# Kernel tuning notes

Hardware: AMD Instinct MI355X
Metric: run time of the kernel (lower is better)

## Reference

```python
import jax, jax.numpy as jnp
import numpy as np

H = 128; L = 4; N_TOTAL = 2500; M = 4; K = 12
S = N_TOTAL * M          # 10000 subgraphs
F = S * K                # 120000 flat nodes
E_INTRA = 2 * F          # 240000 intra-subgraph edges
E_INTER = 16 * N_TOTAL   # 40000 canonical edges
B = 50; VOCAB = 119; MAX_DIST = 32; BN_EPS = 1e-5


def _bn(x, g, b):
    # training-mode BatchNorm1d over rows (biased var, eps=1e-5)
    mu = x.mean(0)
    var = x.var(0)
    return (x - mu) * jax.lax.rsqrt(var + BN_EPS) * g + b


def _gine(x, ei, ea, W1, b1, W2, b2):
    # PyG GINEConv, eps=0: MLP(x + sum_{src->dst} relu(x[src] + e))
    msg = jax.nn.relu(x[ei[0]] + ea)                              # [E,H]
    agg = jax.ops.segment_sum(msg, ei[1], num_segments=x.shape[0])
    h = x + agg
    return jax.nn.relu(h @ W1 + b1) @ W2 + b2


def setup_inputs():
    key = jax.random.key(0)
    ks = list(jax.random.split(key, 32)); it = iter(ks)
    nk = lambda: next(it)
    rn = lambda shape, s=0.05: jax.random.normal(nk(), shape, dtype=jnp.float32) * s
    x_tok = jax.random.randint(nk(), (F,), 0, VOCAB)
    dist = jax.random.randint(nk(), (F,), 0, MAX_DIST + 1)
    node_ids = jax.random.randint(nk(), (F,), 0, N_TOTAL)
    node_ids = jnp.where(jax.random.uniform(nk(), (F,)) < 0.1, -1, node_ids)
    root_flat_idx = jnp.arange(S) * K
    node_ids = node_ids.at[root_flat_idx].set(jnp.arange(S) // M)  # root = canonical node
    valid = node_ids >= 0
    sub_batch = jnp.repeat(jnp.arange(S), K)
    src = jax.random.randint(nk(), (E_INTRA,), 0, F)
    dst = (src // K) * K + jax.random.randint(nk(), (E_INTRA,), 0, K)  # stay inside subgraph
    intra_ei = jnp.stack([src, dst])
    edge_index = jax.random.randint(nk(), (2, E_INTER), 0, N_TOTAL)
    batch_ids = jnp.arange(N_TOTAL) // (N_TOTAL // B)
    lp = -jax.random.uniform(nk(), (S,)) * 3.0                    # log-probs <= 0
    z = lambda *shape: jnp.zeros(shape, jnp.float32)
    o = lambda *shape: jnp.ones(shape, jnp.float32)
    return dict(
        x_tok=x_tok, dist=dist, node_ids=node_ids, valid=valid,
        sub_batch=sub_batch, root_flat_idx=root_flat_idx,
        intra_ei=intra_ei, edge_index=edge_index, batch_ids=batch_ids,
        lp=lp, ea_flat=rn((E_INTRA, H)), edge_attr=rn((E_INTER, H)),
        atom_emb=rn((VOCAB, H)), dist_emb=rn((MAX_DIST + 1, H)),
        logp_w=rn((1, H)), logp_b=z(H),
        intra_W1=rn((L, H, H)), intra_b1=z(L, H),
        intra_W2=rn((L, H, H)), intra_b2=z(L, H),
        intra_bn_g=o(L, H), intra_bn_b=z(L, H),
        self_W=rn((L, H, H)), self_b=z(L, H),
        root_W=rn((L, H, H)), root_b=z(L, H),
        inter_W1=rn((L, H, H)), inter_b1=z(L, H),
        inter_W2=rn((L, H, H)), inter_b2=z(L, H),
        inter_bn_g=o(L, H), inter_bn_b=z(L, H),
        readout_bn_g=o(H), readout_bn_b=z(H),
        alpha_pool=o(1), alpha_inter=o(1),
    )


def reference(x_tok, dist, node_ids, valid, sub_batch, root_flat_idx, intra_ei,
              edge_index, batch_ids, lp, ea_flat, edge_attr, atom_emb, dist_emb,
              logp_w, logp_b, intra_W1, intra_b1, intra_W2, intra_b2,
              intra_bn_g, intra_bn_b, self_W, self_b, root_W, root_b,
              inter_W1, inter_b1, inter_W2, inter_b2, inter_bn_g, inter_bn_b,
              readout_bn_g, readout_bn_b, alpha_pool, alpha_inter):
    valid_f = valid.astype(jnp.float32)[:, None]                  # [F,1]
    is_root_f = jnp.zeros((F, 1), jnp.float32).at[root_flat_idx].set(1.0)
    clamped_ids = jnp.maximum(node_ids, 0)
    # input encoding: atom embedding + BFS-distance PE + log-prob PE
    logp_pe = jax.nn.relu(lp[sub_batch][:, None] * logp_w[0] + logp_b)
    h = (atom_emb[x_tok] + dist_emb[dist] + logp_pe) * valid_f
    # HT inter-root weights, normalized per canonical root id
    root_ids = node_ids[root_flat_idx]                            # [S]
    rv = root_ids >= 0
    rid = jnp.maximum(root_ids, 0)
    w_un = jnp.where(rv, jnp.exp(-alpha_inter[0] * lp), 0.0)
    w_sum = jax.ops.segment_sum(w_un, rid, num_segments=N_TOTAL)
    ht_w = jnp.where(rv, w_un / (w_sum[rid] + 1e-16), 0.0)        # [S]
    for l in range(L):
        h1 = _gine(h, intra_ei, ea_flat, intra_W1[l], intra_b1[l], intra_W2[l], intra_b2[l])
        h1 = _bn(h1, intra_bn_g[l], intra_bn_b[l]) * valid_f
        h_root_bcast = h[sub_batch * K]
        h_non_root = (h @ self_W[l] + self_b[l]) + (h_root_bcast @ root_W[l] + root_b[l])
        # HT-weighted scatter of root reps to canonical nodes
        h_roots = h[root_flat_idx]                                # [S,H]
        h_root_canon = jax.ops.segment_sum(h_roots * ht_w[:, None], rid, num_segments=N_TOTAL)
        h_inter = _gine(h_root_canon, edge_index, edge_attr, inter_W1[l], inter_b1[l], inter_W2[l], inter_b2[l])
        h_inter = _bn(h_inter, inter_bn_g[l], inter_bn_b[l])
        h_inter_bcast = h_inter[clamped_ids] * valid_f
        out = is_root_f * (h1 + h_inter_bcast) + (1.0 - is_root_f) * (h1 + h_non_root)
        h = jax.nn.relu(out) * valid_f                            # dropout p=0
    # HT softmax readout over the m subgraphs of each canonical node
    h_sub = jax.ops.segment_sum(h * valid_f, sub_batch, num_segments=S)
    h_sub_2d = h_sub.reshape(N_TOTAL, M, H)
    w = jax.nn.softmax(-alpha_pool[0] * lp.reshape(N_TOTAL, M), axis=1)
    node_emb = jnp.einsum('nm,nmh->nh', w, h_sub_2d)
    node_emb = _bn(node_emb, readout_bn_g, readout_bn_b)
    return jax.ops.segment_sum(node_emb, batch_ids, num_segments=B)  # [B,H]
```

## Files before the change

### kernel.cpp

```cpp
#include <hip/hip_runtime.h>
#include <math.h>

#define H 128
#define H4 (H/4)
#define KK 12
#define MSUB 4
#define FF 120000
#define SS 10000
#define NN 2500
#define NBATCH 50
#define NLAYER 4
#define EINTRA 240000
#define EINTER 40000
#define HH (H*H)
#define BN_EPS 1e-5f
#define CAP_I 32
#define CAP_E 96

typedef short short8 __attribute__((ext_vector_type(8)));
typedef float floatx4 __attribute__((ext_vector_type(4)));

__device__ __forceinline__ unsigned short f2bf_rne(float x){
  unsigned u = __float_as_uint(x);
  unsigned r = u + 0x7FFFu + ((u >> 16) & 1u);
  return (unsigned short)(r >> 16);
}


__global__ void k_zero(float* __restrict__ p, int n){
  int i = blockIdx.x*256 + threadIdx.x;
  if (i < n) p[i] = 0.f;
}

__global__ void k_zeroi(int* __restrict__ p, int n){
  int i = blockIdx.x*256 + threadIdx.x;
  if (i < n) p[i] = 0;
}


__global__ void k_bucket(const int* __restrict__ dst, int E, int* __restrict__ cnt,
                         int* __restrict__ beid, int cap){
  int e = blockIdx.x*256 + threadIdx.x;
  if (e >= E) return;
  int d = dst[e];
  int p = atomicAdd(&cnt[d], 1);
  if (p < cap) beid[(size_t)d*cap + p] = e;
}


__global__ void k_encode(float* __restrict__ h, const int* __restrict__ xtok,
                         const int* __restrict__ dist, const int* __restrict__ nids,
                         const int* __restrict__ subb, const float* __restrict__ lp,
                         const float* __restrict__ aemb, const float* __restrict__ demb,
                         const float* __restrict__ lw, const float* __restrict__ lb){
  int idx = blockIdx.x*256 + threadIdx.x;
  if (idx >= FF*H4) return;
  int f = idx >> 5; int c = (idx & 31) << 2;
  float vf = (nids[f] >= 0) ? 1.f : 0.f;
  float l = lp[subb[f]];
  float4 a = *(const float4*)(aemb + (size_t)xtok[f]*H + c);
  float4 d = *(const float4*)(demb + (size_t)dist[f]*H + c);
  float4 w = *(const float4*)(lw + c);
  float4 b = *(const float4*)(lb + c);
  float4 o;
  o.x = (a.x + d.x + fmaxf(fmaf(l, w.x, b.x), 0.f)) * vf;
  o.y = (a.y + d.y + fmaxf(fmaf(l, w.y, b.y), 0.f)) * vf;
  o.z = (a.z + d.z + fmaxf(fmaf(l, w.z, b.z), 0.f)) * vf;
  o.w = (a.w + d.w + fmaxf(fmaf(l, w.w, b.w), 0.f)) * vf;
  *(float4*)(h + (size_t)f*H + c) = o;
}


__global__ void k_htw(const int* __restrict__ nids, const int* __restrict__ rfi,
                      const float* __restrict__ lp, const float* __restrict__ alpha,
                      float* __restrict__ htw){
  int n = blockIdx.x*256 + threadIdx.x;
  if (n >= NN) return;
  float a = alpha[0];
  float w[MSUB]; float sum = 0.f;
  #pragma unroll
  for (int m = 0; m < MSUB; ++m){
    int s = n*MSUB + m;
    int rid = nids[rfi[s]];
    float wm = (rid >= 0) ? expf(-a*lp[s]) : 0.f;
    w[m] = wm; sum += wm;
  }
  float inv = 1.f / (sum + 1e-16f);
  #pragma unroll
  for (int m = 0; m < MSUB; ++m) htw[n*MSUB + m] = w[m]*inv;
}


__global__ void k_gine_gather(float* __restrict__ outa, const float* __restrict__ x,
                              const float* __restrict__ ea, const int* __restrict__ cnt,
                              const int* __restrict__ beid, const int* __restrict__ src,
                              int rows, int cap){
  int idx = blockIdx.x*256 + threadIdx.x;
  if (idx >= rows*H4) return;
  int f = idx >> 5; int c = (idx & 31) << 2;
  float4 acc = *(const float4*)(x + (size_t)f*H + c);
  int n = cnt[f]; if (n > cap) n = cap;
  const int* bl = beid + (size_t)f*cap;
  for (int i = 0; i < n; ++i){
    int e = bl[i];
    int s = src[e];
    float4 xv = *(const float4*)(x + (size_t)s*H + c);
    float4 ev = *(const float4*)(ea + (size_t)e*H + c);
    acc.x += fmaxf(xv.x + ev.x, 0.f);
    acc.y += fmaxf(xv.y + ev.y, 0.f);
    acc.z += fmaxf(xv.z + ev.z, 0.f);
    acc.w += fmaxf(xv.w + ev.w, 0.f);
  }
  *(float4*)(outa + (size_t)f*H + c) = acc;
}


__global__ void k_canon(float* __restrict__ canon, const float* __restrict__ h,
                        const float* __restrict__ htw, const int* __restrict__ rfi){
  int idx = blockIdx.x*256 + threadIdx.x;
  if (idx >= NN*H4) return;
  int n = idx >> 5; int c = (idx & 31) << 2;
  float4 acc = make_float4(0.f,0.f,0.f,0.f);
  #pragma unroll
  for (int m = 0; m < MSUB; ++m){
    int s = n*MSUB + m;
    float w = htw[s];
    const float* p = h + (size_t)rfi[s]*H + c;
    acc.x += w*p[0]; acc.y += w*p[1]; acc.z += w*p[2]; acc.w += w*p[3];
  }
  *(float4*)(canon + (size_t)n*H + c) = acc;
}


__global__ __launch_bounds__(256, 2) void k_mm_mfma(
    const float* __restrict__ in, float* __restrict__ out, int rows,
    const float* __restrict__ W, const float* __restrict__ bias,
    int do_relu, const int* __restrict__ gather)
{
  __shared__ __align__(16) short wfrag[2][4][8][64][8];
  int tid = threadIdx.x;
  int w = tid >> 6, l = tid & 63;
  int quad = l >> 4, n15 = l & 15;

  #pragma unroll
  for (int i = 0; i < 8; ++i){
    int c = w + (i << 2);
    int ks = c >> 3, nt = c & 7;
    #pragma unroll
    for (int j = 0; j < 8; ++j){
      int k = ks*32 + quad*8 + j;
      int n = nt*16 + n15;
      float v = W[(size_t)k*H + n];
      unsigned short hb = f2bf_rne(v);
      float hf = __uint_as_float((unsigned)hb << 16);
      unsigned short lb = f2bf_rne(v - hf);
      wfrag[0][ks][nt][l][j] = (short)hb;
      wfrag[1][ks][nt][l][j] = (short)lb;
    }
  }
  __syncthreads();

  int ngroups = (rows + 63) >> 6;
  for (int g = blockIdx.x; g < ngroups; g += gridDim.x){
    int rload = g*64 + w*16 + n15;
    bool okload = rload < rows;
    int ir = okload ? (gather ? gather[rload] : rload) : 0;
    const float* ap = in + (size_t)ir*H + quad*8;

    short8 ah[4], al[4];
    #pragma unroll
    for (int ks = 0; ks < 4; ++ks){
      float4 a0 = okload ? *(const float4*)(ap + ks*32 + 0) : make_float4(0.f,0.f,0.f,0.f);
      float4 a1 = okload ? *(const float4*)(ap + ks*32 + 4) : make_float4(0.f,0.f,0.f,0.f);
      float av[8] = {a0.x,a0.y,a0.z,a0.w,a1.x,a1.y,a1.z,a1.w};
      #pragma unroll
      for (int j = 0; j < 8; ++j){
        unsigned short hb = f2bf_rne(av[j]);
        float hf = __uint_as_float((unsigned)hb << 16);
        ah[ks][j] = (short)hb;
        al[ks][j] = (short)f2bf_rne(av[j] - hf);
      }
    }

    floatx4 acc[8] = {};
    #pragma unroll
    for (int ks = 0; ks < 4; ++ks){
      #pragma unroll
      for (int nt = 0; nt < 8; ++nt){
        short8 bh = *(const short8*)&wfrag[0][ks][nt][l][0];
        short8 bl = *(const short8*)&wfrag[1][ks][nt][l][0];
        acc[nt] = __builtin_amdgcn_mfma_f32_16x16x32_bf16(ah[ks], bh, acc[nt], 0, 0, 0);
        acc[nt] = __builtin_amdgcn_mfma_f32_16x16x32_bf16(al[ks], bh, acc[nt], 0, 0, 0);
        acc[nt] = __builtin_amdgcn_mfma_f32_16x16x32_bf16(ah[ks], bl, acc[nt], 0, 0, 0);
      }
    }

    int rbase = g*64 + w*16 + quad*4;
    #pragma unroll
    for (int nt = 0; nt < 8; ++nt){
      int col = nt*16 + n15;
      float bv = bias[col];
      #pragma unroll
      for (int reg = 0; reg < 4; ++reg){
        int r = rbase + reg;
        if (r < rows){
          float v = acc[nt][reg] + bv;
          if (do_relu) v = fmaxf(v, 0.f);
          out[(size_t)r*H + col] = v;
        }
      }
    }
  }
}


__global__ void k_bnstats(const float* __restrict__ x, int rows, double* __restrict__ stats){
  int g = blockIdx.x*256 + threadIdx.x;
  int c = g & (H-1);
  int rstart = g >> 7;
  int rstride = (gridDim.x*256) >> 7;
  double s = 0.0, s2 = 0.0;
  for (int r = rstart; r < rows; r += rstride){
    float v = x[(size_t)r*H + c];
    s += v; s2 += (double)v*(double)v;
  }
  atomicAdd(&stats[c], s);
  atomicAdd(&stats[H+c], s2);
}

__global__ void k_bnfin(double* __restrict__ stats, int rows, float* __restrict__ muinv){
  int c = threadIdx.x;
  if (c < H){
    double mu = stats[c] / (double)rows;
    double var = stats[H+c] / (double)rows - mu*mu;
    muinv[c]   = (float)mu;
    muinv[H+c] = (float)(1.0 / sqrt(var + (double)BN_EPS));
    stats[c] = 0.0; stats[H+c] = 0.0;
  }
}

__global__ void k_bnapply(float* __restrict__ x, const float* __restrict__ muinv,
                          const float* __restrict__ g, const float* __restrict__ b, int rows){
  int idx = blockIdx.x*256 + threadIdx.x;
  if (idx >= rows*H4) return;
  int r = idx >> 5; int c = (idx & 31) << 2;
  float4 v  = *(const float4*)(x + (size_t)r*H + c);
  float4 mu = *(const float4*)(muinv + c);
  float4 iv = *(const float4*)(muinv + H + c);
  float4 gg = *(const float4*)(g + c);
  float4 bb = *(const float4*)(b + c);
  v.x = (v.x-mu.x)*iv.x*gg.x + bb.x;
  v.y = (v.y-mu.y)*iv.y*gg.y + bb.y;
  v.z = (v.z-mu.z)*iv.z*gg.z + bb.z;
  v.w = (v.w-mu.w)*iv.w*gg.w + bb.w;
  *(float4*)(x + (size_t)r*H + c) = v;
}


__global__ void k_combine(float* __restrict__ h, const float* __restrict__ h1raw,
                          const float* __restrict__ r1, const float* __restrict__ r2,
                          const float* __restrict__ hinter, const float* __restrict__ muinv,
                          const float* __restrict__ bg, const float* __restrict__ bb,
                          const int* __restrict__ nids){
  int idx = blockIdx.x*256 + threadIdx.x;
  if (idx >= FF*H4) return;
  int f = idx >> 5; int c = (idx & 31) << 2;
  int nid = nids[f];
  float vf = (nid >= 0) ? 1.f : 0.f;
  int cid = (nid < 0) ? 0 : nid;
  float4 x  = *(const float4*)(h1raw + (size_t)f*H + c);
  float4 mu = *(const float4*)(muinv + c);
  float4 iv = *(const float4*)(muinv + H + c);
  float4 g4 = *(const float4*)(bg + c);
  float4 b4 = *(const float4*)(bb + c);
  float4 h1;
  h1.x = ((x.x-mu.x)*iv.x*g4.x + b4.x) * vf;
  h1.y = ((x.y-mu.y)*iv.y*g4.y + b4.y) * vf;
  h1.z = ((x.z-mu.z)*iv.z*g4.z + b4.z) * vf;
  h1.w = ((x.w-mu.w)*iv.w*g4.w + b4.w) * vf;
  float4 o;
  if (f % KK == 0){
    float4 hi = *(const float4*)(hinter + (size_t)cid*H + c);
    o.x = h1.x + hi.x*vf; o.y = h1.y + hi.y*vf; o.z = h1.z + hi.z*vf; o.w = h1.w + hi.w*vf;
  } else {
    float4 a  = *(const float4*)(r1 + (size_t)f*H + c);
    float4 rr = *(const float4*)(r2 + (size_t)(f/KK)*H + c);
    o.x = h1.x + a.x + rr.x; o.y = h1.y + a.y + rr.y; o.z = h1.z + a.z + rr.z; o.w = h1.w + a.w + rr.w;
  }
  o.x = fmaxf(o.x,0.f)*vf; o.y = fmaxf(o.y,0.f)*vf; o.z = fmaxf(o.z,0.f)*vf; o.w = fmaxf(o.w,0.f)*vf;
  *(float4*)(h + (size_t)f*H + c) = o;
}


__global__ void k_hsub(float* __restrict__ hsub, const float* __restrict__ h){
  int idx = blockIdx.x*256 + threadIdx.x;
  if (idx >= SS*H4) return;
  int s = idx >> 5; int c = (idx & 31) << 2;
  float4 acc = make_float4(0.f,0.f,0.f,0.f);
  const float* base = h + (size_t)s*KK*H + c;
  #pragma unroll
  for (int k = 0; k < KK; ++k){
    float4 v = *(const float4*)(base + (size_t)k*H);
    acc.x += v.x; acc.y += v.y; acc.z += v.z; acc.w += v.w;
  }
  *(float4*)(hsub + (size_t)s*H + c) = acc;
}

__global__ void k_poolw(float* __restrict__ poolw, const float* __restrict__ lp,
                        const float* __restrict__ alpha){
  int n = blockIdx.x*256 + threadIdx.x;
  if (n >= NN) return;
  float a = alpha[0];
  float s0 = -a*lp[n*MSUB+0], s1 = -a*lp[n*MSUB+1], s2 = -a*lp[n*MSUB+2], s3 = -a*lp[n*MSUB+3];
  float m = fmaxf(fmaxf(s0,s1), fmaxf(s2,s3));
  float e0 = expf(s0-m), e1 = expf(s1-m), e2 = expf(s2-m), e3 = expf(s3-m);
  float sum = e0+e1+e2+e3;
  poolw[n*MSUB+0] = e0/sum; poolw[n*MSUB+1] = e1/sum;
  poolw[n*MSUB+2] = e2/sum; poolw[n*MSUB+3] = e3/sum;
}

__global__ void k_nodeemb(float* __restrict__ nemb, const float* __restrict__ hsub,
                          const float* __restrict__ poolw){
  int idx = blockIdx.x*256 + threadIdx.x;
  if (idx >= NN*H4) return;
  int n = idx >> 5; int c = (idx & 31) << 2;
  float w0 = poolw[n*MSUB+0], w1 = poolw[n*MSUB+1], w2 = poolw[n*MSUB+2], w3 = poolw[n*MSUB+3];
  const float* base = hsub + (size_t)n*MSUB*H + c;
  float4 v0 = *(const float4*)(base + 0*H);
  float4 v1 = *(const float4*)(base + 1*H);
  float4 v2 = *(const float4*)(base + 2*H);
  float4 v3 = *(const float4*)(base + 3*H);
  float4 o;
  o.x = w0*v0.x + w1*v1.x + w2*v2.x + w3*v3.x;
  o.y = w0*v0.y + w1*v1.y + w2*v2.y + w3*v3.y;
  o.z = w0*v0.z + w1*v1.z + w2*v2.z + w3*v3.z;
  o.w = w0*v0.w + w1*v1.w + w2*v2.w + w3*v3.w;
  *(float4*)(nemb + (size_t)n*H + c) = o;
}

__global__ void k_out(float* __restrict__ out, const float* __restrict__ nemb,
                      const float* __restrict__ muinv, const float* __restrict__ g,
                      const float* __restrict__ b){
  int idx = blockIdx.x*256 + threadIdx.x;
  if (idx >= NBATCH*H) return;
  int bi = idx >> 7; int c = idx & (H-1);
  float mu = muinv[c], iv = muinv[H+c], gg = g[c], bb = b[c];
  float acc = 0.f;
  const float* base = nemb + (size_t)bi*(NN/NBATCH)*H + c;
  for (int i = 0; i < NN/NBATCH; ++i)
    acc += (base[(size_t)i*H] - mu)*iv*gg + bb;
  out[idx] = acc;
}


extern "C" void kernel_launch(void* const* d_in, const int* in_sizes, int n_in,
                              void* d_out, int out_size, void* d_ws, size_t ws_size,
                              hipStream_t stream) {
  const int*   x_tok      = (const int*)  d_in[0];
  const int*   dist       = (const int*)  d_in[1];
  const int*   node_ids   = (const int*)  d_in[2];
  const int*   sub_batch  = (const int*)  d_in[4];
  const int*   rfi        = (const int*)  d_in[5];
  const int*   intra_ei   = (const int*)  d_in[6];
  const int*   edge_index = (const int*)  d_in[7];
  const float* lp         = (const float*)d_in[9];
  const float* ea_flat    = (const float*)d_in[10];
  const float* edge_attr  = (const float*)d_in[11];
  const float* atom_emb   = (const float*)d_in[12];
  const float* dist_emb   = (const float*)d_in[13];
  const float* logp_w     = (const float*)d_in[14];
  const float* logp_b     = (const float*)d_in[15];
  const float* intra_W1   = (const float*)d_in[16];
  const float* intra_b1   = (const float*)d_in[17];
  const float* intra_W2   = (const float*)d_in[18];
  const float* intra_b2   = (const float*)d_in[19];
  const float* intra_bn_g = (const float*)d_in[20];
  const float* intra_bn_b = (const float*)d_in[21];
  const float* self_W     = (const float*)d_in[22];
  const float* self_b     = (const float*)d_in[23];
  const float* root_W     = (const float*)d_in[24];
  const float* root_b     = (const float*)d_in[25];
  const float* inter_W1   = (const float*)d_in[26];
  const float* inter_b1   = (const float*)d_in[27];
  const float* inter_W2   = (const float*)d_in[28];
  const float* inter_b2   = (const float*)d_in[29];
  const float* inter_bn_g = (const float*)d_in[30];
  const float* inter_bn_b = (const float*)d_in[31];
  const float* ro_bn_g    = (const float*)d_in[32];
  const float* ro_bn_b    = (const float*)d_in[33];
  const float* alpha_pool = (const float*)d_in[34];
  const float* alpha_inter= (const float*)d_in[35];

  const int* isrc = intra_ei;
  const int* idst = intra_ei + EINTRA;
  const int* esrc = edge_index;
  const int* edst = edge_index + EINTER;

  float* out = (float*)d_out;

  char* ws = (char*)d_ws;
  size_t off = 0;
  auto nxt = [&](size_t bytes) -> void* {
    void* p = ws + off;
    off += (bytes + 255) & ~(size_t)255;
    return p;
  };
  float*  h      = (float*) nxt((size_t)FF*H*4);
  float*  hmid   = (float*) nxt((size_t)FF*H*4);
  float*  tbuf   = (float*) nxt((size_t)FF*H*4);
  float*  r2     = (float*) nxt((size_t)SS*H*4);
  float*  canon  = (float*) nxt((size_t)NN*H*4);
  float*  agg2   = (float*) nxt((size_t)NN*H*4);
  float*  hsub   = (float*) nxt((size_t)SS*H*4);
  float*  nemb   = (float*) nxt((size_t)NN*H*4);
  float*  htw    = (float*) nxt((size_t)SS*4);
  float*  poolw  = (float*) nxt((size_t)NN*MSUB*4);
  double* statsA = (double*)nxt((size_t)2*H*8);
  double* statsB = (double*)nxt((size_t)2*H*8);
  float*  muinvA = (float*) nxt((size_t)2*H*4);
  float*  muinvB = (float*) nxt((size_t)2*H*4);
  int*    icnt   = (int*)   nxt((size_t)FF*4);
  int*    ibeid  = (int*)   nxt((size_t)FF*CAP_I*4);
  int*    ecnt   = (int*)   nxt((size_t)NN*4);
  int*    ebeid  = (int*)   nxt((size_t)NN*CAP_E*4);
  (void)ws_size; (void)n_in; (void)in_sizes; (void)out_size; (void)sub_batch;

  const int G_FH4 = FF*H4/256;
  const int G_SH4 = SS*H4/256;
  const int G_NH4 = (NN*H4 + 255)/256;
  const int G_N   = (NN + 255)/256;
  const int G_MM_F = 512;
  const int G_MM_S = (SS + 63)/64;
  const int G_MM_N = (NN + 63)/64;

  k_zero<<<2, 256, 0, stream>>>((float*)statsA, 2*H*2);
  k_zero<<<2, 256, 0, stream>>>((float*)statsB, 2*H*2);
  k_zeroi<<<(FF+255)/256, 256, 0, stream>>>(icnt, FF);
  k_zeroi<<<G_N, 256, 0, stream>>>(ecnt, NN);

  k_bucket<<<(EINTRA+255)/256, 256, 0, stream>>>(idst, EINTRA, icnt, ibeid, CAP_I);
  k_bucket<<<(EINTER+255)/256, 256, 0, stream>>>(edst, EINTER, ecnt, ebeid, CAP_E);

  k_encode<<<G_FH4, 256, 0, stream>>>(h, x_tok, dist, node_ids, sub_batch, lp,
                                      atom_emb, dist_emb, logp_w, logp_b);
  k_htw<<<G_N, 256, 0, stream>>>(node_ids, rfi, lp, alpha_inter, htw);

  for (int l = 0; l < NLAYER; ++l){
    const float* W1 = intra_W1 + (size_t)l*HH; const float* b1 = intra_b1 + (size_t)l*H;
    const float* W2 = intra_W2 + (size_t)l*HH; const float* b2 = intra_b2 + (size_t)l*H;

    k_gine_gather<<<G_FH4, 256, 0, stream>>>(hmid, h, ea_flat, icnt, ibeid, isrc, FF, CAP_I);
    k_mm_mfma<<<G_MM_F, 256, 0, stream>>>(hmid, tbuf, FF, W1, b1, 1, nullptr);
    k_mm_mfma<<<G_MM_F, 256, 0, stream>>>(tbuf, hmid, FF, W2, b2, 0, nullptr);
    k_bnstats<<<512, 256, 0, stream>>>(hmid, FF, statsA);
    k_bnfin<<<1, 128, 0, stream>>>(statsA, FF, muinvA);

    k_canon<<<G_NH4, 256, 0, stream>>>(canon, h, htw, rfi);
    k_mm_mfma<<<G_MM_S, 256, 0, stream>>>(h, r2, SS, root_W + (size_t)l*HH,
                                          root_b + (size_t)l*H, 0, rfi);

    k_gine_gather<<<G_NH4, 256, 0, stream>>>(agg2, canon, edge_attr, ecnt, ebeid, esrc, NN, CAP_E);
    k_mm_mfma<<<G_MM_N, 256, 0, stream>>>(agg2, tbuf, NN, inter_W1 + (size_t)l*HH,
                                          inter_b1 + (size_t)l*H, 1, nullptr);
    k_mm_mfma<<<G_MM_N, 256, 0, stream>>>(tbuf, agg2, NN, inter_W2 + (size_t)l*HH,
                                          inter_b2 + (size_t)l*H, 0, nullptr);
    k_bnstats<<<128, 256, 0, stream>>>(agg2, NN, statsB);
    k_bnfin<<<1, 128, 0, stream>>>(statsB, NN, muinvB);
    k_bnapply<<<G_NH4, 256, 0, stream>>>(agg2, muinvB, inter_bn_g + (size_t)l*H,
                                         inter_bn_b + (size_t)l*H, NN);

    k_mm_mfma<<<G_MM_F, 256, 0, stream>>>(h, tbuf, FF, self_W + (size_t)l*HH,
                                          self_b + (size_t)l*H, 0, nullptr);
    k_combine<<<G_FH4, 256, 0, stream>>>(h, hmid, tbuf, r2, agg2, muinvA,
                                         intra_bn_g + (size_t)l*H,
                                         intra_bn_b + (size_t)l*H, node_ids);
  }

  k_hsub<<<G_SH4, 256, 0, stream>>>(hsub, h);
  k_poolw<<<G_N, 256, 0, stream>>>(poolw, lp, alpha_pool);
  k_nodeemb<<<G_NH4, 256, 0, stream>>>(nemb, hsub, poolw);
  k_bnstats<<<128, 256, 0, stream>>>(nemb, NN, statsB);
  k_bnfin<<<1, 128, 0, stream>>>(statsB, NN, muinvB);
  k_out<<<(NBATCH*H+255)/256, 256, 0, stream>>>(out, nemb, muinvB, ro_bn_g, ro_bn_b);
}
```

Before: 2.017 ms.

## Fuse self-matmul with combine epilogue and compact edge lists into CSR pairs

```diff
diff --git a/kernel.cpp b/kernel.cpp
--- a/kernel.cpp
+++ b/kernel.cpp
@@ -45,6 +45,41 @@
   int d = dst[e];
   int p = atomicAdd(&cnt[d], 1);
   if (p < cap) beid[(size_t)d*cap + p] = e;
+}
+
+__global__ void k_scan(const int* __restrict__ cnt, int rows, int cap,
+                       int* __restrict__ rowptr, int* __restrict__ gcount){
+  __shared__ int sdata[256];
+  __shared__ int sbase;
+  int tid = threadIdx.x;
+  int r = blockIdx.x*256 + tid;
+  int v = 0;
+  if (r < rows){ v = cnt[r]; if (v > cap) v = cap; }
+  sdata[tid] = v;
+  __syncthreads();
+  for (int ofs = 1; ofs < 256; ofs <<= 1){
+    int t = (tid >= ofs) ? sdata[tid-ofs] : 0;
+    __syncthreads();
+    sdata[tid] += t;
+    __syncthreads();
+  }
+  if (tid == 255) sbase = atomicAdd(gcount, sdata[255]);
+  __syncthreads();
+  if (r < rows) rowptr[r] = sbase + sdata[tid] - v;
+}
+
+__global__ void k_csr_fill(const int* __restrict__ cnt, const int* __restrict__ rowptr,
+                           const int* __restrict__ beid, const int* __restrict__ src,
+                           int rows, int cap, int2* __restrict__ es){
+  int f = blockIdx.x*256 + threadIdx.x;
+  if (f >= rows) return;
+  int n = cnt[f]; if (n > cap) n = cap;
+  int base = rowptr[f];
+  const int* bl = beid + (size_t)f*cap;
+  for (int i = 0; i < n; ++i){
+    int e = bl[i];
+    es[base + i] = make_int2(e, src[e]);
+  }
 }
 
 
@@ -91,25 +126,37 @@
 }
 
 
-__global__ void k_gine_gather(float* __restrict__ outa, const float* __restrict__ x,
-                              const float* __restrict__ ea, const int* __restrict__ cnt,
-                              const int* __restrict__ beid, const int* __restrict__ src,
-                              int rows, int cap){
+__global__ void k_gine_gather2(float* __restrict__ outa, const float* __restrict__ x,
+                               const float* __restrict__ ea, const int* __restrict__ cnt,
+                               const int* __restrict__ rowptr, const int2* __restrict__ es,
+                               int rows, int cap){
   int idx = blockIdx.x*256 + threadIdx.x;
   if (idx >= rows*H4) return;
   int f = idx >> 5; int c = (idx & 31) << 2;
   float4 acc = *(const float4*)(x + (size_t)f*H + c);
   int n = cnt[f]; if (n > cap) n = cap;
-  const int* bl = beid + (size_t)f*cap;
-  for (int i = 0; i < n; ++i){
-    int e = bl[i];
-    int s = src[e];
-    float4 xv = *(const float4*)(x + (size_t)s*H + c);
-    float4 ev = *(const float4*)(ea + (size_t)e*H + c);
-    acc.x += fmaxf(xv.x + ev.x, 0.f);
-    acc.y += fmaxf(xv.y + ev.y, 0.f);
-    acc.z += fmaxf(xv.z + ev.z, 0.f);
-    acc.w += fmaxf(xv.w + ev.w, 0.f);
+  const int2* p = es + rowptr[f];
+  int i = 0;
+  for (; i + 2 <= n; i += 2){
+    int2 e0 = p[i];
+    int2 e1 = p[i+1];
+    float4 x0 = *(const float4*)(x + (size_t)e0.y*H + c);
+    float4 a0 = *(const float4*)(ea + (size_t)e0.x*H + c);
+    float4 x1 = *(const float4*)(x + (size_t)e1.y*H + c);
+    float4 a1 = *(const float4*)(ea + (size_t)e1.x*H + c);
+    acc.x += fmaxf(x0.x + a0.x, 0.f) + fmaxf(x1.x + a1.x, 0.f);
+    acc.y += fmaxf(x0.y + a0.y, 0.f) + fmaxf(x1.y + a1.y, 0.f);
+    acc.z += fmaxf(x0.z + a0.z, 0.f) + fmaxf(x1.z + a1.z, 0.f);
+    acc.w += fmaxf(x0.w + a0.w, 0.f) + fmaxf(x1.w + a1.w, 0.f);
+  }
+  if (i < n){
+    int2 e0 = p[i];
+    float4 x0 = *(const float4*)(x + (size_t)e0.y*H + c);
+    float4 a0 = *(const float4*)(ea + (size_t)e0.x*H + c);
+    acc.x += fmaxf(x0.x + a0.x, 0.f);
+    acc.y += fmaxf(x0.y + a0.y, 0.f);
+    acc.z += fmaxf(x0.z + a0.z, 0.f);
+    acc.w += fmaxf(x0.w + a0.w, 0.f);
   }
   *(float4*)(outa + (size_t)f*H + c) = acc;
 }
@@ -207,6 +254,99 @@
           float v = acc[nt][reg] + bv;
           if (do_relu) v = fmaxf(v, 0.f);
           out[(size_t)r*H + col] = v;
+        }
+      }
+    }
+  }
+}
+
+
+__global__ __launch_bounds__(256, 2) void k_mm_combine(
+    const float* in, float* hout, int rows,
+    const float* __restrict__ W, const float* __restrict__ bias,
+    const float* __restrict__ hmid, const float* __restrict__ r2,
+    const float* __restrict__ hinter, const float* __restrict__ muinv,
+    const float* __restrict__ bng, const float* __restrict__ bnb,
+    const int* __restrict__ nids)
+{
+  __shared__ __align__(16) short wfrag[2][4][8][64][8];
+  int tid = threadIdx.x;
+  int w = tid >> 6, l = tid & 63;
+  int quad = l >> 4, n15 = l & 15;
+
+  #pragma unroll
+  for (int i = 0; i < 8; ++i){
+    int c = w + (i << 2);
+    int ks = c >> 3, nt = c & 7;
+    #pragma unroll
+    for (int j = 0; j < 8; ++j){
+      int k = ks*32 + quad*8 + j;
+      int n = nt*16 + n15;
+      float v = W[(size_t)k*H + n];
+      unsigned short hb = f2bf_rne(v);
+      float hf = __uint_as_float((unsigned)hb << 16);
+      unsigned short lb = f2bf_rne(v - hf);
+      wfrag[0][ks][nt][l][j] = (short)hb;
+      wfrag[1][ks][nt][l][j] = (short)lb;
+    }
+  }
+  __syncthreads();
+
+  int ngroups = (rows + 63) >> 6;
+  for (int g = blockIdx.x; g < ngroups; g += gridDim.x){
+    int rload = g*64 + w*16 + n15;
+    bool okload = rload < rows;
+    const float* ap = in + (size_t)(okload ? rload : 0)*H + quad*8;
+
+    short8 ah[4], al[4];
+    #pragma unroll
+    for (int ks = 0; ks < 4; ++ks){
+      float4 a0 = okload ? *(const float4*)(ap + ks*32 + 0) : make_float4(0.f,0.f,0.f,0.f);
+      float4 a1 = okload ? *(const float4*)(ap + ks*32 + 4) : make_float4(0.f,0.f,0.f,0.f);
+      float av[8] = {a0.x,a0.y,a0.z,a0.w,a1.x,a1.y,a1.z,a1.w};
+      #pragma unroll
+      for (int j = 0; j < 8; ++j){
+        unsigned short hb = f2bf_rne(av[j]);
+        float hf = __uint_as_float((unsigned)hb << 16);
+        ah[ks][j] = (short)hb;
+        al[ks][j] = (short)f2bf_rne(av[j] - hf);
+      }
+    }
+
+    floatx4 acc[8] = {};
+    #pragma unroll
+    for (int ks = 0; ks < 4; ++ks){
+      #pragma unroll
+      for (int nt = 0; nt < 8; ++nt){
+        short8 bh = *(const short8*)&wfrag[0][ks][nt][l][0];
+        short8 bl = *(const short8*)&wfrag[1][ks][nt][l][0];
+        acc[nt] = __builtin_amdgcn_mfma_f32_16x16x32_bf16(ah[ks], bh, acc[nt], 0, 0, 0);
+        acc[nt] = __builtin_amdgcn_mfma_f32_16x16x32_bf16(al[ks], bh, acc[nt], 0, 0, 0);
+        acc[nt] = __builtin_amdgcn_mfma_f32_16x16x32_bf16(ah[ks], bl, acc[nt], 0, 0, 0);
+      }
+    }
+
+    int rbase = g*64 + w*16 + quad*4;
+    #pragma unroll
+    for (int reg = 0; reg < 4; ++reg){
+      int r = rbase + reg;
+      if (r < rows){
+        int nid = nids[r];
+        float vf = (nid >= 0) ? 1.f : 0.f;
+        int cid = (nid < 0) ? 0 : nid;
+        bool isroot = (r % KK) == 0;
+        const float* hmrow = hmid + (size_t)r*H;
+        const float* r2row = r2 + (size_t)(r/KK)*H;
+        const float* hirow = hinter + (size_t)cid*H;
+        float* orow = hout + (size_t)r*H;
+        #pragma unroll
+        for (int nt = 0; nt < 8; ++nt){
+          int col = nt*16 + n15;
+          float h1 = ((hmrow[col] - muinv[col]) * muinv[H+col] * bng[col] + bnb[col]) * vf;
+          float o;
+          if (isroot) o = h1 + hirow[col] * vf;
+          else        o = h1 + (acc[nt][reg] + bias[col]) + r2row[col];
+          orow[col] = fmaxf(o, 0.f) * vf;
         }
       }
     }
@@ -254,41 +394,6 @@
   v.z = (v.z-mu.z)*iv.z*gg.z + bb.z;
   v.w = (v.w-mu.w)*iv.w*gg.w + bb.w;
   *(float4*)(x + (size_t)r*H + c) = v;
-}
-
-
-__global__ void k_combine(float* __restrict__ h, const float* __restrict__ h1raw,
-                          const float* __restrict__ r1, const float* __restrict__ r2,
-                          const float* __restrict__ hinter, const float* __restrict__ muinv,
-                          const float* __restrict__ bg, const float* __restrict__ bb,
-                          const int* __restrict__ nids){
-  int idx = blockIdx.x*256 + threadIdx.x;
-  if (idx >= FF*H4) return;
-  int f = idx >> 5; int c = (idx & 31) << 2;
-  int nid = nids[f];
-  float vf = (nid >= 0) ? 1.f : 0.f;
-  int cid = (nid < 0) ? 0 : nid;
-  float4 x  = *(const float4*)(h1raw + (size_t)f*H + c);
-  float4 mu = *(const float4*)(muinv + c);
-  float4 iv = *(const float4*)(muinv + H + c);
-  float4 g4 = *(const float4*)(bg + c);
-  float4 b4 = *(const float4*)(bb + c);
-  float4 h1;
-  h1.x = ((x.x-mu.x)*iv.x*g4.x + b4.x) * vf;
-  h1.y = ((x.y-mu.y)*iv.y*g4.y + b4.y) * vf;
-  h1.z = ((x.z-mu.z)*iv.z*g4.z + b4.z) * vf;
-  h1.w = ((x.w-mu.w)*iv.w*g4.w + b4.w) * vf;
-  float4 o;
-  if (f % KK == 0){
-    float4 hi = *(const float4*)(hinter + (size_t)cid*H + c);
-    o.x = h1.x + hi.x*vf; o.y = h1.y + hi.y*vf; o.z = h1.z + hi.z*vf; o.w = h1.w + hi.w*vf;
-  } else {
-    float4 a  = *(const float4*)(r1 + (size_t)f*H + c);
-    float4 rr = *(const float4*)(r2 + (size_t)(f/KK)*H + c);
-    o.x = h1.x + a.x + rr.x; o.y = h1.y + a.y + rr.y; o.z = h1.z + a.z + rr.z; o.w = h1.w + a.w + rr.w;
-  }
-  o.x = fmaxf(o.x,0.f)*vf; o.y = fmaxf(o.y,0.f)*vf; o.z = fmaxf(o.z,0.f)*vf; o.w = fmaxf(o.w,0.f)*vf;
-  *(float4*)(h + (size_t)f*H + c) = o;
 }
 
 
@@ -423,23 +528,34 @@
   int*    ibeid  = (int*)   nxt((size_t)FF*CAP_I*4);
   int*    ecnt   = (int*)   nxt((size_t)NN*4);
   int*    ebeid  = (int*)   nxt((size_t)NN*CAP_E*4);
+  int*    irow   = (int*)   nxt((size_t)FF*4);
+  int*    erow   = (int*)   nxt((size_t)NN*4);
+  int2*   ies    = (int2*)  nxt((size_t)EINTRA*8);
+  int2*   ees    = (int2*)  nxt((size_t)EINTER*8);
+  int*    gcnt   = (int*)   nxt((size_t)2*4);
   (void)ws_size; (void)n_in; (void)in_sizes; (void)out_size; (void)sub_batch;
 
   const int G_FH4 = FF*H4/256;
   const int G_SH4 = SS*H4/256;
   const int G_NH4 = (NN*H4 + 255)/256;
   const int G_N   = (NN + 255)/256;
+  const int G_F   = (FF + 255)/256;
   const int G_MM_F = 512;
   const int G_MM_S = (SS + 63)/64;
   const int G_MM_N = (NN + 63)/64;
 
   k_zero<<<2, 256, 0, stream>>>((float*)statsA, 2*H*2);
   k_zero<<<2, 256, 0, stream>>>((float*)statsB, 2*H*2);
-  k_zeroi<<<(FF+255)/256, 256, 0, stream>>>(icnt, FF);
+  k_zeroi<<<G_F, 256, 0, stream>>>(icnt, FF);
   k_zeroi<<<G_N, 256, 0, stream>>>(ecnt, NN);
+  k_zeroi<<<1, 256, 0, stream>>>(gcnt, 2);
 
   k_bucket<<<(EINTRA+255)/256, 256, 0, stream>>>(idst, EINTRA, icnt, ibeid, CAP_I);
   k_bucket<<<(EINTER+255)/256, 256, 0, stream>>>(edst, EINTER, ecnt, ebeid, CAP_E);
+  k_scan<<<G_F, 256, 0, stream>>>(icnt, FF, CAP_I, irow, gcnt);
+  k_scan<<<G_N, 256, 0, stream>>>(ecnt, NN, CAP_E, erow, gcnt+1);
+  k_csr_fill<<<G_F, 256, 0, stream>>>(icnt, irow, ibeid, isrc, FF, CAP_I, ies);
+  k_csr_fill<<<G_N, 256, 0, stream>>>(ecnt, erow, ebeid, esrc, NN, CAP_E, ees);
 
   k_encode<<<G_FH4, 256, 0, stream>>>(h, x_tok, dist, node_ids, sub_batch, lp,
                                       atom_emb, dist_emb, logp_w, logp_b);
@@ -449,7 +565,7 @@
     const float* W1 = intra_W1 + (size_t)l*HH; const float* b1 = intra_b1 + (size_t)l*H;
     const float* W2 = intra_W2 + (size_t)l*HH; const float* b2 = intra_b2 + (size_t)l*H;
 
-    k_gine_gather<<<G_FH4, 256, 0, stream>>>(hmid, h, ea_flat, icnt, ibeid, isrc, FF, CAP_I);
+    k_gine_gather2<<<G_FH4, 256, 0, stream>>>(hmid, h, ea_flat, icnt, irow, ies, FF, CAP_I);
     k_mm_mfma<<<G_MM_F, 256, 0, stream>>>(hmid, tbuf, FF, W1, b1, 1, nullptr);
     k_mm_mfma<<<G_MM_F, 256, 0, stream>>>(tbuf, hmid, FF, W2, b2, 0, nullptr);
     k_bnstats<<<512, 256, 0, stream>>>(hmid, FF, statsA);
@@ -459,7 +575,7 @@
     k_mm_mfma<<<G_MM_S, 256, 0, stream>>>(h, r2, SS, root_W + (size_t)l*HH,
                                           root_b + (size_t)l*H, 0, rfi);
 
-    k_gine_gather<<<G_NH4, 256, 0, stream>>>(agg2, canon, edge_attr, ecnt, ebeid, esrc, NN, CAP_E);
+    k_gine_gather2<<<G_NH4, 256, 0, stream>>>(agg2, canon, edge_attr, ecnt, erow, ees, NN, CAP_E);
     k_mm_mfma<<<G_MM_N, 256, 0, stream>>>(agg2, tbuf, NN, inter_W1 + (size_t)l*HH,
                                           inter_b1 + (size_t)l*H, 1, nullptr);
     k_mm_mfma<<<G_MM_N, 256, 0, stream>>>(tbuf, agg2, NN, inter_W2 + (size_t)l*HH,
@@ -469,11 +585,10 @@
     k_bnapply<<<G_NH4, 256, 0, stream>>>(agg2, muinvB, inter_bn_g + (size_t)l*H,
                                          inter_bn_b + (size_t)l*H, NN);
 
-    k_mm_mfma<<<G_MM_F, 256, 0, stream>>>(h, tbuf, FF, self_W + (size_t)l*HH,
-                                          self_b + (size_t)l*H, 0, nullptr);
-    k_combine<<<G_FH4, 256, 0, stream>>>(h, hmid, tbuf, r2, agg2, muinvA,
-                                         intra_bn_g + (size_t)l*H,
-                                         intra_bn_b + (size_t)l*H, node_ids);
+    k_mm_combine<<<G_MM_F, 256, 0, stream>>>(h, h, FF, self_W + (size_t)l*HH,
+                                             self_b + (size_t)l*H, hmid, r2, agg2,
+                                             muinvA, intra_bn_g + (size_t)l*H,
+                                             intra_bn_b + (size_t)l*H, node_ids);
   }
 
   k_hsub<<<G_SH4, 256, 0, stream>>>(hsub, h);
```

New measurement: 2.201 ms. 9.1% more time.
